# Performance work log

Measured on AMD Instinct MI355X. Metric: run time of the kernel, lower is better.

## Reference

```python
import jax, jax.numpy as jnp
import numpy as np

N = 100000      # nodes
E = 1600000     # edges (unique, no self-loops)
DIN = 128
DOUT = 128


def _make_edges():
    """Unique undirected edges, no self-loops, ring guarantees min degree 2.
    Ensures dense-adjacency semantics == edge-list segment-sum semantics."""
    rng = np.random.default_rng(0)
    ring = np.stack([np.arange(N, dtype=np.int64), (np.arange(N, dtype=np.int64) + 1) % N], axis=1)
    ring = np.sort(ring, axis=1)  # canonical (min,max)
    ring_keys = ring[:, 0] * N + ring[:, 1]
    cand = rng.integers(0, N, size=(3 * E, 2), dtype=np.int64)
    cand = cand[cand[:, 0] != cand[:, 1]]
    cand = np.sort(cand, axis=1)
    keys = cand[:, 0] * N + cand[:, 1]
    _, idx = np.unique(keys, return_index=True)
    cand = cand[np.sort(idx)]
    cand = cand[~np.isin(cand[:, 0] * N + cand[:, 1], ring_keys)][: E - N]
    edges = np.concatenate([ring, cand], axis=0)  # [E, 2]
    return edges.T  # [2, E]


def setup_inputs() -> dict:
    key = jax.random.key(0)
    kx, kw = jax.random.split(key)
    X = jax.random.normal(kx, (N, DIN), dtype=jnp.float32)
    # kaiming_normal_ default (fan_in mode): std = sqrt(2 / fan_in)
    W = jax.random.normal(kw, (DIN, DOUT), dtype=jnp.float32) * np.float32(np.sqrt(2.0 / DIN))
    edge_list = jnp.asarray(_make_edges(), dtype=jnp.int64)
    return {"X": X, "W": W, "edge_list": edge_list}


def reference(X, W, edge_list):
    src, dst = edge_list[0], edge_list[1]
    n = X.shape[0]
    ones = jnp.ones(src.shape[0], dtype=X.dtype)
    # D: each edge increments both endpoint degrees (matches the torch loop)
    deg = jnp.zeros((n,), X.dtype).at[src].add(ones).at[dst].add(ones)
    # A_hat @ X = symmetric neighbor aggregation + self (identity)
    agg = jnp.zeros_like(X).at[dst].add(X[src]).at[src].add(X[dst]) + X
    # D^-1 is inverse of diagonal -> elementwise reciprocal
    z = (agg / deg[:, None]) @ W
    return jax.nn.relu(z)
```

## Files before the change

kernel.cpp:

```cpp
#include <hip/hip_runtime.h>
#include <hip/hip_fp16.h>


#define DFEAT 128
#define BSH 7
#define BNODES (1 << BSH)
#define NBMAX 800
#define EPB 8192
#define SORT_CAP 6144

typedef __attribute__((ext_vector_type(8))) short short8;
typedef __attribute__((ext_vector_type(4))) float f32x4;

__device__ __forceinline__ unsigned short f2bf(float x) {
  unsigned u = __float_as_uint(x);
  return (unsigned short)((u + 0x7FFFu + ((u >> 16) & 1u)) >> 16);
}
__device__ __forceinline__ __half2 u2h(unsigned x) {
  union { unsigned u; __half2 h; } c; c.u = x; return c.h;
}

__global__ void init_kernel(const int* el32, int* gcur, int* flag, int NB) {
  int i = blockIdx.x * blockDim.x + threadIdx.x;
  if (i < NB) gcur[i] = 0;
  if (i == 0) flag[0] = (el32[1] == 0 && el32[3] == 0) ? 1 : 0;
}

__device__ __forceinline__ int edge_at(const void* el, long long i, int mode64) {
  if (mode64) return (int)((const long long*)el)[i];
  return ((const int*)el)[i];
}

__global__ __launch_bounds__(1024) void scatter_kernel(const void* el,
                                                       const int* __restrict__ flag,
                                                       int* __restrict__ gcur,
                                                       unsigned int* __restrict__ bucket,
                                                       int E, int NB) {
  __shared__ int lh[NBMAX];
  __shared__ int lb[NBMAX];
  int t = threadIdx.x;
  for (int i = t; i < NB; i += 1024) lh[i] = 0;
  __syncthreads();
  int m = flag[0];
  long long e0 = (long long)blockIdx.x * EPB + t;
  int s[8], d[8];
#pragma unroll
  for (int r = 0; r < 8; r++) {
    long long e = e0 + r * 1024;
    if (e < E) {
      s[r] = edge_at(el, e, m);
      d[r] = edge_at(el, (long long)E + e, m);
    } else {
      s[r] = -1;
    }
  }
#pragma unroll
  for (int r = 0; r < 8; r++) {
    if (s[r] >= 0) {
      atomicAdd(&lh[s[r] >> BSH], 1);
      atomicAdd(&lh[d[r] >> BSH], 1);
    }
  }
  __syncthreads();
  for (int i = t; i < NB; i += 1024) {
    int c = lh[i];
    lb[i] = c ? atomicAdd(&gcur[i], c) : 0;
  }
  __syncthreads();
  for (int i = t; i < NB; i += 1024) lh[i] = 0;
  __syncthreads();
#pragma unroll
  for (int r = 0; r < 8; r++) {
    if (s[r] >= 0) {
      int bs = s[r] >> BSH, bd = d[r] >> BSH;
      int ps = lb[bs] + atomicAdd(&lh[bs], 1);
      if (ps < SORT_CAP)
        bucket[(long long)bs * SORT_CAP + ps] =
            ((unsigned)(s[r] & (BNODES - 1)) << 20) | (unsigned)d[r];
      int pd = lb[bd] + atomicAdd(&lh[bd], 1);
      if (pd < SORT_CAP)
        bucket[(long long)bd * SORT_CAP + pd] =
            ((unsigned)(d[r] & (BNODES - 1)) << 20) | (unsigned)s[r];
    }
  }
}

__global__ __launch_bounds__(1024) void sort_kernel(const unsigned int* __restrict__ bucket,
                                                    const int* __restrict__ gcur,
                                                    int* __restrict__ adj,
                                                    int* __restrict__ start,
                                                    int* __restrict__ degg,
                                                    int n) {
  __shared__ int srt[SORT_CAP];
  __shared__ int h[BNODES], pref[BNODES], cur[BNODES], scn[BNODES];
  int b = blockIdx.x, t = threadIdx.x;
  int cnt = gcur[b]; if (cnt > SORT_CAP) cnt = SORT_CAP;
  long long base = (long long)b * SORT_CAP;

  if (t < BNODES) h[t] = 0;
  __syncthreads();
  for (int i = t; i < cnt; i += 1024)
    atomicAdd(&h[bucket[base + i] >> 20], 1);
  __syncthreads();
  int v = (t < BNODES) ? h[t] : 0;
  if (t < BNODES) scn[t] = v;
  __syncthreads();
  for (int dd = 1; dd < BNODES; dd <<= 1) {
    int a = (t < BNODES && t >= dd) ? scn[t - dd] : 0;
    __syncthreads();
    if (t < BNODES) scn[t] += a;
    __syncthreads();
  }
  if (t < BNODES) { pref[t] = scn[t] - v; cur[t] = scn[t] - v; }
  __syncthreads();
  for (int i = t; i < cnt; i += 1024) {
    unsigned e = bucket[base + i];
    int p = atomicAdd(&cur[e >> 20], 1);
    srt[p] = (int)(e & 0xFFFFFu);
  }
  __syncthreads();
  for (int i = t; i < cnt; i += 1024) adj[base + i] = srt[i];
  int node = (b << BSH) + t;
  if (t < BNODES && node < n) {
    start[node] = (int)(base + pref[t]);
    degg[node] = h[t];
  }
}

__global__ __launch_bounds__(256) void wfrag_kernel(const float* __restrict__ W,
                                                    unsigned int* __restrict__ Wfrag) {
  int e = blockIdx.x * 256 + threadIdx.x;
  if (e >= 2048) return;
  int lane = e & 63;
  int nt = (e >> 6) & 7;
  int kc = e >> 9;
  int k0 = kc * 32 + (lane >> 4) * 8;
  int col = nt * 16 + (lane & 15);
  unsigned int o[4];
#pragma unroll
  for (int jj = 0; jj < 4; jj++) {
    unsigned short lo = f2bf(W[(k0 + 2 * jj) * DFEAT + col]);
    unsigned short hi = f2bf(W[(k0 + 2 * jj + 1) * DFEAT + col]);
    o[jj] = (unsigned)lo | ((unsigned)hi << 16);
  }
  uint4* dst = (uint4*)Wfrag;
  uint4 v; v.x = o[0]; v.y = o[1]; v.z = o[2]; v.w = o[3];
  dst[e] = v;
}

__global__ __launch_bounds__(256) void gemm_kernel(const float* __restrict__ X,
                                                   const short8* __restrict__ Wfrag,
                                                   __half* __restrict__ Yh, int n) {
  int wave = threadIdx.x >> 6;
  int lane = threadIdx.x & 63;
  int row0 = (blockIdx.x * 4 + wave) * 16;
  if (row0 >= n) return;

  int rowA = row0 + (lane & 15);
  if (rowA >= n) rowA = n - 1;
  const float4* Xrow = (const float4*)(X + (long long)rowA * DFEAT);
  int koff = (lane >> 4) * 2;

  f32x4 acc[8];
#pragma unroll
  for (int ntp = 0; ntp < 8; ntp++) acc[ntp] = (f32x4){0.f, 0.f, 0.f, 0.f};

#pragma unroll
  for (int kc = 0; kc < 4; kc++) {
    float4 xa = Xrow[kc * 8 + koff];
    float4 xb = Xrow[kc * 8 + koff + 1];
    short8 a8;
    a8[0] = (short)f2bf(xa.x); a8[1] = (short)f2bf(xa.y);
    a8[2] = (short)f2bf(xa.z); a8[3] = (short)f2bf(xa.w);
    a8[4] = (short)f2bf(xb.x); a8[5] = (short)f2bf(xb.y);
    a8[6] = (short)f2bf(xb.z); a8[7] = (short)f2bf(xb.w);
#pragma unroll
    for (int nt = 0; nt < 8; nt++) {
      short8 b8 = Wfrag[(kc * 8 + nt) * 64 + lane];
      acc[nt] = __builtin_amdgcn_mfma_f32_16x16x32_bf16(a8, b8, acc[nt], 0, 0, 0);
    }
  }

  int rbase = row0 + (lane >> 4) * 4;
  int cbase = lane & 15;
#pragma unroll
  for (int nt = 0; nt < 8; nt++) {
#pragma unroll
    for (int r = 0; r < 4; r++) {
      int row = rbase + r;
      if (row < n)
        Yh[(long long)row * DFEAT + nt * 16 + cbase] = __float2half(acc[nt][r]);
    }
  }
}

__global__ __launch_bounds__(256) void gather_kernel(const unsigned int* __restrict__ Yh,
                                                     const int* __restrict__ start,
                                                     const int* __restrict__ degg,
                                                     const int* __restrict__ adj,
                                                     float2* __restrict__ out2, int n) {
  int wid = (int)((blockIdx.x * (long long)blockDim.x + threadIdx.x) >> 6);
  int lane = threadIdx.x & 63;
  if (wid >= n) return;

  int off0 = start[wid], len = degg[wid];
  __half2 acc0 = u2h(Yh[(long long)wid * 64 + lane]);
  __half2 acc1 = u2h(0);

  for (int base = 0; base < len; base += 64) {
    int cnt = len - base; if (cnt > 64) cnt = 64;
    int idx = (lane < cnt) ? adj[off0 + base + lane] : 0;
    int t = 0;
    for (; t + 8 <= cnt; t += 8) {
      unsigned v[8];
#pragma unroll
      for (int u = 0; u < 8; u++) {
        int j = __shfl(idx, t + u);
        v[u] = Yh[(long long)j * 64 + lane];
      }
      acc0 = __hadd2(acc0, u2h(v[0])); acc1 = __hadd2(acc1, u2h(v[1]));
      acc0 = __hadd2(acc0, u2h(v[2])); acc1 = __hadd2(acc1, u2h(v[3]));
      acc0 = __hadd2(acc0, u2h(v[4])); acc1 = __hadd2(acc1, u2h(v[5]));
      acc0 = __hadd2(acc0, u2h(v[6])); acc1 = __hadd2(acc1, u2h(v[7]));
    }
    for (; t < cnt; t++) {
      int j = __shfl(idx, t);
      acc0 = __hadd2(acc0, u2h(Yh[(long long)j * 64 + lane]));
    }
  }

  float2 f0 = __half22float2(acc0);
  float2 f1 = __half22float2(acc1);
  float inv = 1.0f / (float)len;
  float2 o;
  o.x = (f0.x + f1.x) * inv;
  o.y = (f0.y + f1.y) * inv;
  o.x = o.x > 0.f ? o.x : 0.f;
  o.y = o.y > 0.f ? o.y : 0.f;
  out2[(long long)wid * 64 + lane] = o;
}

extern "C" void kernel_launch(void* const* d_in, const int* in_sizes, int n_in,
                              void* d_out, int out_size, void* d_ws, size_t ws_size,
                              hipStream_t stream) {
  const float* X = (const float*)d_in[0];
  const float* W = (const float*)d_in[1];
  const void* el = d_in[2];
  float* out = (float*)d_out;

  int n = in_sizes[0] / DFEAT;
  int E = in_sizes[2] / 2;
  int NB = (n + BNODES - 1) >> BSH;

  char* p = (char*)d_ws;
  auto alloc = [&](size_t bytes) -> char* {
    char* q = p;
    p += (bytes + 511) & ~(size_t)511;
    return q;
  };
  int* gcur = (int*)alloc((size_t)NBMAX * 4);
  int* flag = (int*)alloc(64);
  unsigned int* bucket = (unsigned int*)alloc((size_t)NBMAX * SORT_CAP * 4);
  int* adj   = (int*)alloc((size_t)NBMAX * SORT_CAP * 4);
  int* start = (int*)alloc((size_t)n * 4);
  int* degg  = (int*)alloc((size_t)n * 4);
  unsigned int* Wfrag = (unsigned int*)alloc((size_t)2048 * 16);
  __half* Yh = (__half*)alloc((size_t)n * DFEAT * 2);

  int eblocks = (E + EPB - 1) / EPB;

  init_kernel<<<(NBMAX + 255) / 256, 256, 0, stream>>>((const int*)el, gcur, flag, NB);
  scatter_kernel<<<eblocks, 1024, 0, stream>>>(el, flag, gcur, bucket, E, NB);
  sort_kernel<<<NB, 1024, 0, stream>>>(bucket, gcur, adj, start, degg, n);
  wfrag_kernel<<<8, 256, 0, stream>>>(W, Wfrag);
  gemm_kernel<<<(n + 63) / 64, 256, 0, stream>>>(X, (const short8*)Wfrag, Yh, n);
  gather_kernel<<<(n + 3) / 4, 256, 0, stream>>>((const unsigned int*)Yh, start, degg,
                                                 adj, (float2*)out, n);
}
```

Before: 267.0 us.

## Split Y into feature slices and gather per slice for cache locality

The GEMM now writes Y as eight feature-sliced planes of 16 halfs per row instead of row-major 128-wide rows. The gather runs eight passes, one per slice, with each wave handling 8 neighbors at a time across lane groups and then reducing with cross-lane shuffles. The aim is to shrink the random-access working set per pass (each plane is 3.2 MB) so neighbor rows stay in L2/MALL. In exchange it reads 32-byte segments instead of 256-byte rows, rereads adjacency and degree data eight times, and adds shuffle reductions.

```diff
diff --git a/kernel.cpp b/kernel.cpp
--- a/kernel.cpp
+++ b/kernel.cpp
@@ -8,6 +8,8 @@
 #define NBMAX 800
 #define EPB 8192
 #define SORT_CAP 6144
+#define NSLICE 8
+#define SFEAT 16
 
 typedef __attribute__((ext_vector_type(8))) short short8;
 typedef __attribute__((ext_vector_type(4))) float f32x4;
@@ -18,6 +20,9 @@
 }
 __device__ __forceinline__ __half2 u2h(unsigned x) {
   union { unsigned u; __half2 h; } c; c.u = x; return c.h;
+}
+__device__ __forceinline__ unsigned h2u(__half2 x) {
+  union { __half2 h; unsigned u; } c; c.h = x; return c.u;
 }
 
 __global__ void init_kernel(const int* el32, int* gcur, int* flag, int NB) {
@@ -185,11 +190,12 @@
   int cbase = lane & 15;
 #pragma unroll
   for (int nt = 0; nt < 8; nt++) {
+    __half* Ys = Yh + (long long)nt * n * SFEAT;
 #pragma unroll
     for (int r = 0; r < 4; r++) {
       int row = rbase + r;
       if (row < n)
-        Yh[(long long)row * DFEAT + nt * 16 + cbase] = __float2half(acc[nt][r]);
+        Ys[(long long)row * SFEAT + cbase] = __float2half(acc[nt][r]);
     }
   }
 }
@@ -198,46 +204,60 @@
                                                      const int* __restrict__ start,
                                                      const int* __restrict__ degg,
                                                      const int* __restrict__ adj,
-                                                     float2* __restrict__ out2, int n) {
-  int wid = (int)((blockIdx.x * (long long)blockDim.x + threadIdx.x) >> 6);
+                                                     float* __restrict__ out,
+                                                     int n, int bps) {
+  int slice = blockIdx.x / bps;
+  int nb = blockIdx.x % bps;
+  int wave = threadIdx.x >> 6;
+  int wid = nb * 4 + wave;
+  if (wid >= n) return;
   int lane = threadIdx.x & 63;
-  if (wid >= n) return;
-
+  int g = lane >> 3, fl = lane & 7;
+
+  const unsigned int* Ys = Yh + (long long)slice * n * (SFEAT / 2);
   int off0 = start[wid], len = degg[wid];
-  __half2 acc0 = u2h(Yh[(long long)wid * 64 + lane]);
+
+  __half2 acc0 = u2h(g == 0 ? Ys[(long long)wid * 8 + fl] : 0u);
   __half2 acc1 = u2h(0);
 
   for (int base = 0; base < len; base += 64) {
     int cnt = len - base; if (cnt > 64) cnt = 64;
     int idx = (lane < cnt) ? adj[off0 + base + lane] : 0;
     int t = 0;
-    for (; t + 8 <= cnt; t += 8) {
-      unsigned v[8];
-#pragma unroll
-      for (int u = 0; u < 8; u++) {
-        int j = __shfl(idx, t + u);
-        v[u] = Yh[(long long)j * 64 + lane];
-      }
-      acc0 = __hadd2(acc0, u2h(v[0])); acc1 = __hadd2(acc1, u2h(v[1]));
-      acc0 = __hadd2(acc0, u2h(v[2])); acc1 = __hadd2(acc1, u2h(v[3]));
-      acc0 = __hadd2(acc0, u2h(v[4])); acc1 = __hadd2(acc1, u2h(v[5]));
-      acc0 = __hadd2(acc0, u2h(v[6])); acc1 = __hadd2(acc1, u2h(v[7]));
-    }
-    for (; t < cnt; t++) {
-      int j = __shfl(idx, t);
-      acc0 = __hadd2(acc0, u2h(Yh[(long long)j * 64 + lane]));
-    }
-  }
-
-  float2 f0 = __half22float2(acc0);
-  float2 f1 = __half22float2(acc1);
-  float inv = 1.0f / (float)len;
-  float2 o;
-  o.x = (f0.x + f1.x) * inv;
-  o.y = (f0.y + f1.y) * inv;
-  o.x = o.x > 0.f ? o.x : 0.f;
-  o.y = o.y > 0.f ? o.y : 0.f;
-  out2[(long long)wid * 64 + lane] = o;
+    for (; t + 32 <= cnt; t += 32) {
+      int j0 = __shfl(idx, t + g);
+      int j1 = __shfl(idx, t + 8 + g);
+      int j2 = __shfl(idx, t + 16 + g);
+      int j3 = __shfl(idx, t + 24 + g);
+      unsigned u0 = Ys[(long long)j0 * 8 + fl];
+      unsigned u1 = Ys[(long long)j1 * 8 + fl];
+      unsigned u2 = Ys[(long long)j2 * 8 + fl];
+      unsigned u3 = Ys[(long long)j3 * 8 + fl];
+      acc0 = __hadd2(acc0, u2h(u0)); acc1 = __hadd2(acc1, u2h(u1));
+      acc0 = __hadd2(acc0, u2h(u2)); acc1 = __hadd2(acc1, u2h(u3));
+    }
+    for (; t < cnt; t += 8) {
+      int j = __shfl(idx, t + g);
+      unsigned u = Ys[(long long)j * 8 + fl];
+      if (t + g < cnt) acc0 = __hadd2(acc0, u2h(u));
+    }
+  }
+
+  __half2 acc = __hadd2(acc0, acc1);
+  acc = __hadd2(acc, u2h((unsigned)__shfl_xor((int)h2u(acc), 8)));
+  acc = __hadd2(acc, u2h((unsigned)__shfl_xor((int)h2u(acc), 16)));
+  acc = __hadd2(acc, u2h((unsigned)__shfl_xor((int)h2u(acc), 32)));
+
+  if (g == 0) {
+    float2 f = __half22float2(acc);
+    float inv = 1.0f / (float)len;
+    float2 o;
+    o.x = f.x * inv; o.y = f.y * inv;
+    o.x = o.x > 0.f ? o.x : 0.f;
+    o.y = o.y > 0.f ? o.y : 0.f;
+    float2* op = (float2*)(out + (long long)wid * DFEAT + slice * SFEAT);
+    op[fl] = o;
+  }
 }
 
 extern "C" void kernel_launch(void* const* d_in, const int* in_sizes, int n_in,
@@ -268,12 +288,13 @@
   __half* Yh = (__half*)alloc((size_t)n * DFEAT * 2);
 
   int eblocks = (E + EPB - 1) / EPB;
+  int bps = (n + 3) / 4;
 
   init_kernel<<<(NBMAX + 255) / 256, 256, 0, stream>>>((const int*)el, gcur, flag, NB);
   scatter_kernel<<<eblocks, 1024, 0, stream>>>(el, flag, gcur, bucket, E, NB);
   sort_kernel<<<NB, 1024, 0, stream>>>(bucket, gcur, adj, start, degg, n);
   wfrag_kernel<<<8, 256, 0, stream>>>(W, Wfrag);
   gemm_kernel<<<(n + 63) / 64, 256, 0, stream>>>(X, (const short8*)Wfrag, Yh, n);
-  gather_kernel<<<(n + 3) / 4, 256, 0, stream>>>((const unsigned int*)Yh, start, degg,
-                                                 adj, (float2*)out, n);
-}
+  gather_kernel<<<bps * NSLICE, 256, 0, stream>>>((const unsigned int*)Yh, start, degg,
+                                                  adj, out, n, bps);
+}
```

Result: slower. 412.8 us (+54.6%).

## Privatize LDS histograms per sub-group in scatter/sort and fuse W prep into init

Applied to the files above, without the earlier changes.

Splits the shared-memory bucket histograms in the scatter and sort kernels into four per-subgroup copies, which cuts LDS atomic contention, and assigns per-subgroup offsets so the ordering stays consistent. The sort kernel now uses 512 threads and caches bucket entries in LDS so they are read from global memory only once. The W-to-bf16 fragment conversion is merged into the init kernel, saving one launch. In exchange, the scatter kernel issues four times as many global atomicAdds on the bucket counters, and both kernels use more LDS.

```diff
diff --git a/kernel.cpp b/kernel.cpp
--- a/kernel.cpp
+++ b/kernel.cpp
@@ -8,6 +8,7 @@
 #define NBMAX 800
 #define EPB 8192
 #define SORT_CAP 6144
+#define NSUB 4
 
 typedef __attribute__((ext_vector_type(8))) short short8;
 typedef __attribute__((ext_vector_type(4))) float f32x4;
@@ -20,10 +21,28 @@
   union { unsigned u; __half2 h; } c; c.u = x; return c.h;
 }
 
-__global__ void init_kernel(const int* el32, int* gcur, int* flag, int NB) {
-  int i = blockIdx.x * blockDim.x + threadIdx.x;
-  if (i < NB) gcur[i] = 0;
-  if (i == 0) flag[0] = (el32[1] == 0 && el32[3] == 0) ? 1 : 0;
+__global__ __launch_bounds__(256) void setup_kernel(const int* el32,
+                                                    const float* __restrict__ W,
+                                                    int* gcur, int* flag,
+                                                    unsigned int* __restrict__ Wfrag) {
+  int id = blockIdx.x * 256 + threadIdx.x;
+  if (id < NBMAX) gcur[id] = 0;
+  if (id == 0) flag[0] = (el32[1] == 0 && el32[3] == 0) ? 1 : 0;
+
+  int lane = id & 63;
+  int nt = (id >> 6) & 7;
+  int kc = id >> 9;
+  int k0 = kc * 32 + (lane >> 4) * 8;
+  int col = nt * 16 + (lane & 15);
+  unsigned int o[4];
+#pragma unroll
+  for (int jj = 0; jj < 4; jj++) {
+    unsigned short lo = f2bf(W[(k0 + 2 * jj) * DFEAT + col]);
+    unsigned short hi = f2bf(W[(k0 + 2 * jj + 1) * DFEAT + col]);
+    o[jj] = (unsigned)lo | ((unsigned)hi << 16);
+  }
+  uint4 v; v.x = o[0]; v.y = o[1]; v.z = o[2]; v.w = o[3];
+  ((uint4*)Wfrag)[id] = v;
 }
 
 __device__ __forceinline__ int edge_at(const void* el, long long i, int mode64) {
@@ -36,10 +55,11 @@
                                                        int* __restrict__ gcur,
                                                        unsigned int* __restrict__ bucket,
                                                        int E, int NB) {
-  __shared__ int lh[NBMAX];
-  __shared__ int lb[NBMAX];
+  __shared__ int lh[NSUB][NBMAX];
+  __shared__ int lb[NSUB][NBMAX];
   int t = threadIdx.x;
-  for (int i = t; i < NB; i += 1024) lh[i] = 0;
+  int sub = t >> 8;
+  for (int i = t; i < NSUB * NBMAX; i += 1024) (&lh[0][0])[i] = 0;
   __syncthreads();
   int m = flag[0];
   long long e0 = (long long)blockIdx.x * EPB + t;
@@ -57,27 +77,30 @@
 #pragma unroll
   for (int r = 0; r < 8; r++) {
     if (s[r] >= 0) {
-      atomicAdd(&lh[s[r] >> BSH], 1);
-      atomicAdd(&lh[d[r] >> BSH], 1);
-    }
-  }
-  __syncthreads();
-  for (int i = t; i < NB; i += 1024) {
-    int c = lh[i];
-    lb[i] = c ? atomicAdd(&gcur[i], c) : 0;
-  }
-  __syncthreads();
-  for (int i = t; i < NB; i += 1024) lh[i] = 0;
+      atomicAdd(&lh[sub][s[r] >> BSH], 1);
+      atomicAdd(&lh[sub][d[r] >> BSH], 1);
+    }
+  }
+  __syncthreads();
+  for (int i = t; i < NSUB * NB; i += 1024) {
+    int ss = i >> 10;
+    ss = i / NB;
+    int bb = i - ss * NB;
+    int c = lh[ss][bb];
+    lb[ss][bb] = c ? atomicAdd(&gcur[bb], c) : 0;
+  }
+  __syncthreads();
+  for (int i = t; i < NSUB * NBMAX; i += 1024) (&lh[0][0])[i] = 0;
   __syncthreads();
 #pragma unroll
   for (int r = 0; r < 8; r++) {
     if (s[r] >= 0) {
       int bs = s[r] >> BSH, bd = d[r] >> BSH;
-      int ps = lb[bs] + atomicAdd(&lh[bs], 1);
+      int ps = lb[sub][bs] + atomicAdd(&lh[sub][bs], 1);
       if (ps < SORT_CAP)
         bucket[(long long)bs * SORT_CAP + ps] =
             ((unsigned)(s[r] & (BNODES - 1)) << 20) | (unsigned)d[r];
-      int pd = lb[bd] + atomicAdd(&lh[bd], 1);
+      int pd = lb[sub][bd] + atomicAdd(&lh[sub][bd], 1);
       if (pd < SORT_CAP)
         bucket[(long long)bd * SORT_CAP + pd] =
             ((unsigned)(d[r] & (BNODES - 1)) << 20) | (unsigned)s[r];
@@ -85,25 +108,35 @@
   }
 }
 
-__global__ __launch_bounds__(1024) void sort_kernel(const unsigned int* __restrict__ bucket,
-                                                    const int* __restrict__ gcur,
-                                                    int* __restrict__ adj,
-                                                    int* __restrict__ start,
-                                                    int* __restrict__ degg,
-                                                    int n) {
+__global__ __launch_bounds__(512) void sort_kernel(const unsigned int* __restrict__ bucket,
+                                                   const int* __restrict__ gcur,
+                                                   int* __restrict__ adj,
+                                                   int* __restrict__ start,
+                                                   int* __restrict__ degg,
+                                                   int n) {
+  __shared__ unsigned ent[SORT_CAP];
   __shared__ int srt[SORT_CAP];
-  __shared__ int h[BNODES], pref[BNODES], cur[BNODES], scn[BNODES];
+  __shared__ int h[NSUB][BNODES];
+  __shared__ int tot[BNODES], pref[BNODES], scn[BNODES];
+  __shared__ int cur[NSUB][BNODES];
   int b = blockIdx.x, t = threadIdx.x;
+  int sub = t >> 7;
   int cnt = gcur[b]; if (cnt > SORT_CAP) cnt = SORT_CAP;
   long long base = (long long)b * SORT_CAP;
 
-  if (t < BNODES) h[t] = 0;
-  __syncthreads();
-  for (int i = t; i < cnt; i += 1024)
-    atomicAdd(&h[bucket[base + i] >> 20], 1);
-  __syncthreads();
-  int v = (t < BNODES) ? h[t] : 0;
-  if (t < BNODES) scn[t] = v;
+  for (int i = t; i < NSUB * BNODES; i += 512) (&h[0][0])[i] = 0;
+  __syncthreads();
+  for (int i = t; i < cnt; i += 512) {
+    unsigned e = bucket[base + i];
+    ent[i] = e;
+    atomicAdd(&h[sub][e >> 20], 1);
+  }
+  __syncthreads();
+  if (t < BNODES) {
+    int s0 = h[0][t], s1 = h[1][t], s2 = h[2][t], s3 = h[3][t];
+    tot[t] = s0 + s1 + s2 + s3;
+    scn[t] = tot[t];
+  }
   __syncthreads();
   for (int dd = 1; dd < BNODES; dd <<= 1) {
     int a = (t < BNODES && t >= dd) ? scn[t - dd] : 0;
@@ -111,41 +144,27 @@
     if (t < BNODES) scn[t] += a;
     __syncthreads();
   }
-  if (t < BNODES) { pref[t] = scn[t] - v; cur[t] = scn[t] - v; }
-  __syncthreads();
-  for (int i = t; i < cnt; i += 1024) {
-    unsigned e = bucket[base + i];
-    int p = atomicAdd(&cur[e >> 20], 1);
+  if (t < BNODES) {
+    int ex = scn[t] - tot[t];
+    pref[t] = ex;
+    cur[0][t] = ex;
+    cur[1][t] = ex + h[0][t];
+    cur[2][t] = ex + h[0][t] + h[1][t];
+    cur[3][t] = ex + h[0][t] + h[1][t] + h[2][t];
+  }
+  __syncthreads();
+  for (int i = t; i < cnt; i += 512) {
+    unsigned e = ent[i];
+    int p = atomicAdd(&cur[sub][e >> 20], 1);
     srt[p] = (int)(e & 0xFFFFFu);
   }
   __syncthreads();
-  for (int i = t; i < cnt; i += 1024) adj[base + i] = srt[i];
+  for (int i = t; i < cnt; i += 512) adj[base + i] = srt[i];
   int node = (b << BSH) + t;
   if (t < BNODES && node < n) {
     start[node] = (int)(base + pref[t]);
-    degg[node] = h[t];
-  }
-}
-
-__global__ __launch_bounds__(256) void wfrag_kernel(const float* __restrict__ W,
-                                                    unsigned int* __restrict__ Wfrag) {
-  int e = blockIdx.x * 256 + threadIdx.x;
-  if (e >= 2048) return;
-  int lane = e & 63;
-  int nt = (e >> 6) & 7;
-  int kc = e >> 9;
-  int k0 = kc * 32 + (lane >> 4) * 8;
-  int col = nt * 16 + (lane & 15);
-  unsigned int o[4];
-#pragma unroll
-  for (int jj = 0; jj < 4; jj++) {
-    unsigned short lo = f2bf(W[(k0 + 2 * jj) * DFEAT + col]);
-    unsigned short hi = f2bf(W[(k0 + 2 * jj + 1) * DFEAT + col]);
-    o[jj] = (unsigned)lo | ((unsigned)hi << 16);
-  }
-  uint4* dst = (uint4*)Wfrag;
-  uint4 v; v.x = o[0]; v.y = o[1]; v.z = o[2]; v.w = o[3];
-  dst[e] = v;
+    degg[node] = tot[t];
+  }
 }
 
 __global__ __launch_bounds__(256) void gemm_kernel(const float* __restrict__ X,
@@ -269,10 +288,9 @@
 
   int eblocks = (E + EPB - 1) / EPB;
 
-  init_kernel<<<(NBMAX + 255) / 256, 256, 0, stream>>>((const int*)el, gcur, flag, NB);
+  setup_kernel<<<8, 256, 0, stream>>>((const int*)el, W, gcur, flag, Wfrag);
   scatter_kernel<<<eblocks, 1024, 0, stream>>>(el, flag, gcur, bucket, E, NB);
-  sort_kernel<<<NB, 1024, 0, stream>>>(bucket, gcur, adj, start, degg, n);
-  wfrag_kernel<<<8, 256, 0, stream>>>(W, Wfrag);
+  sort_kernel<<<NB, 512, 0, stream>>>(bucket, gcur, adj, start, degg, n);
   gemm_kernel<<<(n + 63) / 64, 256, 0, stream>>>(X, (const short8*)Wfrag, Yh, n);
   gather_kernel<<<(n + 3) / 4, 256, 0, stream>>>((const unsigned int*)Yh, start, degg,
                                                  adj, (float2*)out, n);
```

After: 270.7 us. No clear change (+1.4%).

## Fuse W-fragment prep into init and co-schedule sort with GEMM blocks

Applied to the files above, without the earlier changes.

Folds W bf16 fragment packing into the init kernel, and merges the per-bucket sort and the X·W MFMA GEMM into one launch, with separate block ranges so both run concurrently. The sort now stages entries in LDS and writes adj directly instead of through a sorted LDS copy, and uses 512 threads. The gather is split into three launches over node ranges. This cuts launch count and lets the compute-bound GEMM overlap the latency-bound sort. The three-way gather split adds launches with no clear benefit, and the direct scattered adj writes may coalesce worse.

```diff
diff --git a/kernel.cpp b/kernel.cpp
--- a/kernel.cpp
+++ b/kernel.cpp
@@ -20,10 +20,28 @@
   union { unsigned u; __half2 h; } c; c.u = x; return c.h;
 }
 
-__global__ void init_kernel(const int* el32, int* gcur, int* flag, int NB) {
-  int i = blockIdx.x * blockDim.x + threadIdx.x;
-  if (i < NB) gcur[i] = 0;
-  if (i == 0) flag[0] = (el32[1] == 0 && el32[3] == 0) ? 1 : 0;
+__global__ __launch_bounds__(256) void setup_kernel(const int* el32,
+                                                    const float* __restrict__ W,
+                                                    int* gcur, int* flag,
+                                                    unsigned int* __restrict__ Wfrag) {
+  int id = blockIdx.x * 256 + threadIdx.x;
+  if (id < NBMAX) gcur[id] = 0;
+  if (id == 0) flag[0] = (el32[1] == 0 && el32[3] == 0) ? 1 : 0;
+
+  int lane = id & 63;
+  int nt = (id >> 6) & 7;
+  int kc = id >> 9;
+  int k0 = kc * 32 + (lane >> 4) * 8;
+  int col = nt * 16 + (lane & 15);
+  unsigned int o[4];
+#pragma unroll
+  for (int jj = 0; jj < 4; jj++) {
+    unsigned short lo = f2bf(W[(k0 + 2 * jj) * DFEAT + col]);
+    unsigned short hi = f2bf(W[(k0 + 2 * jj + 1) * DFEAT + col]);
+    o[jj] = (unsigned)lo | ((unsigned)hi << 16);
+  }
+  uint4 v; v.x = o[0]; v.y = o[1]; v.z = o[2]; v.w = o[3];
+  ((uint4*)Wfrag)[id] = v;
 }
 
 __device__ __forceinline__ int edge_at(const void* el, long long i, int mode64) {
@@ -85,111 +103,90 @@
   }
 }
 
-__global__ __launch_bounds__(1024) void sort_kernel(const unsigned int* __restrict__ bucket,
-                                                    const int* __restrict__ gcur,
-                                                    int* __restrict__ adj,
-                                                    int* __restrict__ start,
-                                                    int* __restrict__ degg,
-                                                    int n) {
-  __shared__ int srt[SORT_CAP];
+__global__ __launch_bounds__(512) void sortgemm_kernel(
+    const unsigned int* __restrict__ bucket, const int* __restrict__ gcur,
+    int* __restrict__ adj, int* __restrict__ start, int* __restrict__ degg,
+    const float* __restrict__ X, const short8* __restrict__ Wfrag,
+    __half* __restrict__ Yh, int n, int NB) {
+  __shared__ unsigned ent[SORT_CAP];
   __shared__ int h[BNODES], pref[BNODES], cur[BNODES], scn[BNODES];
-  int b = blockIdx.x, t = threadIdx.x;
-  int cnt = gcur[b]; if (cnt > SORT_CAP) cnt = SORT_CAP;
-  long long base = (long long)b * SORT_CAP;
-
-  if (t < BNODES) h[t] = 0;
-  __syncthreads();
-  for (int i = t; i < cnt; i += 1024)
-    atomicAdd(&h[bucket[base + i] >> 20], 1);
-  __syncthreads();
-  int v = (t < BNODES) ? h[t] : 0;
-  if (t < BNODES) scn[t] = v;
-  __syncthreads();
-  for (int dd = 1; dd < BNODES; dd <<= 1) {
-    int a = (t < BNODES && t >= dd) ? scn[t - dd] : 0;
-    __syncthreads();
-    if (t < BNODES) scn[t] += a;
-    __syncthreads();
-  }
-  if (t < BNODES) { pref[t] = scn[t] - v; cur[t] = scn[t] - v; }
-  __syncthreads();
-  for (int i = t; i < cnt; i += 1024) {
-    unsigned e = bucket[base + i];
-    int p = atomicAdd(&cur[e >> 20], 1);
-    srt[p] = (int)(e & 0xFFFFFu);
-  }
-  __syncthreads();
-  for (int i = t; i < cnt; i += 1024) adj[base + i] = srt[i];
-  int node = (b << BSH) + t;
-  if (t < BNODES && node < n) {
-    start[node] = (int)(base + pref[t]);
-    degg[node] = h[t];
-  }
-}
-
-__global__ __launch_bounds__(256) void wfrag_kernel(const float* __restrict__ W,
-                                                    unsigned int* __restrict__ Wfrag) {
-  int e = blockIdx.x * 256 + threadIdx.x;
-  if (e >= 2048) return;
-  int lane = e & 63;
-  int nt = (e >> 6) & 7;
-  int kc = e >> 9;
-  int k0 = kc * 32 + (lane >> 4) * 8;
-  int col = nt * 16 + (lane & 15);
-  unsigned int o[4];
-#pragma unroll
-  for (int jj = 0; jj < 4; jj++) {
-    unsigned short lo = f2bf(W[(k0 + 2 * jj) * DFEAT + col]);
-    unsigned short hi = f2bf(W[(k0 + 2 * jj + 1) * DFEAT + col]);
-    o[jj] = (unsigned)lo | ((unsigned)hi << 16);
-  }
-  uint4* dst = (uint4*)Wfrag;
-  uint4 v; v.x = o[0]; v.y = o[1]; v.z = o[2]; v.w = o[3];
-  dst[e] = v;
-}
-
-__global__ __launch_bounds__(256) void gemm_kernel(const float* __restrict__ X,
-                                                   const short8* __restrict__ Wfrag,
-                                                   __half* __restrict__ Yh, int n) {
-  int wave = threadIdx.x >> 6;
-  int lane = threadIdx.x & 63;
-  int row0 = (blockIdx.x * 4 + wave) * 16;
-  if (row0 >= n) return;
-
-  int rowA = row0 + (lane & 15);
-  if (rowA >= n) rowA = n - 1;
-  const float4* Xrow = (const float4*)(X + (long long)rowA * DFEAT);
-  int koff = (lane >> 4) * 2;
-
-  f32x4 acc[8];
-#pragma unroll
-  for (int ntp = 0; ntp < 8; ntp++) acc[ntp] = (f32x4){0.f, 0.f, 0.f, 0.f};
-
-#pragma unroll
-  for (int kc = 0; kc < 4; kc++) {
-    float4 xa = Xrow[kc * 8 + koff];
-    float4 xb = Xrow[kc * 8 + koff + 1];
-    short8 a8;
-    a8[0] = (short)f2bf(xa.x); a8[1] = (short)f2bf(xa.y);
-    a8[2] = (short)f2bf(xa.z); a8[3] = (short)f2bf(xa.w);
-    a8[4] = (short)f2bf(xb.x); a8[5] = (short)f2bf(xb.y);
-    a8[6] = (short)f2bf(xb.z); a8[7] = (short)f2bf(xb.w);
+
+  if ((int)blockIdx.x < NB) {
+    int b = blockIdx.x, t = threadIdx.x;
+    int cnt = gcur[b]; if (cnt > SORT_CAP) cnt = SORT_CAP;
+    long long base = (long long)b * SORT_CAP;
+
+    if (t < BNODES) h[t] = 0;
+    __syncthreads();
+    for (int i = t; i < cnt; i += 512) {
+      unsigned e = bucket[base + i];
+      ent[i] = e;
+      atomicAdd(&h[e >> 20], 1);
+    }
+    __syncthreads();
+    int v = (t < BNODES) ? h[t] : 0;
+    if (t < BNODES) scn[t] = v;
+    __syncthreads();
+    for (int dd = 1; dd < BNODES; dd <<= 1) {
+      int a = (t < BNODES && t >= dd) ? scn[t - dd] : 0;
+      __syncthreads();
+      if (t < BNODES) scn[t] += a;
+      __syncthreads();
+    }
+    if (t < BNODES) { pref[t] = scn[t] - v; cur[t] = scn[t] - v; }
+    __syncthreads();
+    for (int i = t; i < cnt; i += 512) {
+      unsigned e = ent[i];
+      int p = atomicAdd(&cur[e >> 20], 1);
+      adj[base + p] = (int)(e & 0xFFFFFu);
+    }
+    int node = (b << BSH) + t;
+    if (t < BNODES && node < n) {
+      start[node] = (int)(base + pref[t]);
+      degg[node] = h[t];
+    }
+  } else {
+    int gb = blockIdx.x - NB;
+    int wave = threadIdx.x >> 6;
+    int lane = threadIdx.x & 63;
+    int row0 = (gb * 8 + wave) * 16;
+    if (row0 >= n) return;
+
+    int rowA = row0 + (lane & 15);
+    if (rowA >= n) rowA = n - 1;
+    const float4* Xrow = (const float4*)(X + (long long)rowA * DFEAT);
+    int koff = (lane >> 4) * 2;
+
+    f32x4 acc[8];
+#pragma unroll
+    for (int ntp = 0; ntp < 8; ntp++) acc[ntp] = (f32x4){0.f, 0.f, 0.f, 0.f};
+
+#pragma unroll
+    for (int kc = 0; kc < 4; kc++) {
+      float4 xa = Xrow[kc * 8 + koff];
+      float4 xb = Xrow[kc * 8 + koff + 1];
+      short8 a8;
+      a8[0] = (short)f2bf(xa.x); a8[1] = (short)f2bf(xa.y);
+      a8[2] = (short)f2bf(xa.z); a8[3] = (short)f2bf(xa.w);
+      a8[4] = (short)f2bf(xb.x); a8[5] = (short)f2bf(xb.y);
+      a8[6] = (short)f2bf(xb.z); a8[7] = (short)f2bf(xb.w);
+#pragma unroll
+      for (int nt = 0; nt < 8; nt++) {
+        short8 b8 = Wfrag[(kc * 8 + nt) * 64 + lane];
+        acc[nt] = __builtin_amdgcn_mfma_f32_16x16x32_bf16(a8, b8, acc[nt], 0, 0, 0);
+      }
+    }
+
+    int rbase = row0 + (lane >> 4) * 4;
+    int cbase = lane & 15;
 #pragma unroll
     for (int nt = 0; nt < 8; nt++) {
-      short8 b8 = Wfrag[(kc * 8 + nt) * 64 + lane];
-      acc[nt] = __builtin_amdgcn_mfma_f32_16x16x32_bf16(a8, b8, acc[nt], 0, 0, 0);
-    }
-  }
-
-  int rbase = row0 + (lane >> 4) * 4;
-  int cbase = lane & 15;
-#pragma unroll
-  for (int nt = 0; nt < 8; nt++) {
-#pragma unroll
-    for (int r = 0; r < 4; r++) {
-      int row = rbase + r;
-      if (row < n)
-        Yh[(long long)row * DFEAT + nt * 16 + cbase] = __float2half(acc[nt][r]);
+#pragma unroll
+      for (int r = 0; r < 4; r++) {
+        int row = rbase + r;
+        if (row < n)
+          Yh[(long long)row * DFEAT + nt * 16 + cbase] = __float2half(acc[nt][r]);
+      }
     }
   }
 }
@@ -198,10 +195,11 @@
                                                      const int* __restrict__ start,
                                                      const int* __restrict__ degg,
                                                      const int* __restrict__ adj,
-                                                     float2* __restrict__ out2, int n) {
-  int wid = (int)((blockIdx.x * (long long)blockDim.x + threadIdx.x) >> 6);
+                                                     float2* __restrict__ out2,
+                                                     int nbeg, int nend) {
+  int wid = nbeg + (int)((blockIdx.x * (long long)blockDim.x + threadIdx.x) >> 6);
   int lane = threadIdx.x & 63;
-  if (wid >= n) return;
+  if (wid >= nend) return;
 
   int off0 = start[wid], len = degg[wid];
   __half2 acc0 = u2h(Yh[(long long)wid * 64 + lane]);
@@ -268,12 +266,19 @@
   __half* Yh = (__half*)alloc((size_t)n * DFEAT * 2);
 
   int eblocks = (E + EPB - 1) / EPB;
-
-  init_kernel<<<(NBMAX + 255) / 256, 256, 0, stream>>>((const int*)el, gcur, flag, NB);
+  int gemmblocks = (n + 127) / 128;
+
+  setup_kernel<<<8, 256, 0, stream>>>((const int*)el, W, gcur, flag, Wfrag);
   scatter_kernel<<<eblocks, 1024, 0, stream>>>(el, flag, gcur, bucket, E, NB);
-  sort_kernel<<<NB, 1024, 0, stream>>>(bucket, gcur, adj, start, degg, n);
-  wfrag_kernel<<<8, 256, 0, stream>>>(W, Wfrag);
-  gemm_kernel<<<(n + 63) / 64, 256, 0, stream>>>(X, (const short8*)Wfrag, Yh, n);
-  gather_kernel<<<(n + 3) / 4, 256, 0, stream>>>((const unsigned int*)Yh, start, degg,
-                                                 adj, (float2*)out, n);
-}
+  sortgemm_kernel<<<NB + gemmblocks, 512, 0, stream>>>(
+      bucket, gcur, adj, start, degg, X, (const short8*)Wfrag, Yh, n, NB);
+
+  int np = (n + 2) / 3;
+  for (int k = 0; k < 3; k++) {
+    int nbeg = k * np;
+    int nend = (k == 2) ? n : (k + 1) * np;
+    int blocks = ((nend - nbeg) + 3) / 4;
+    gather_kernel<<<blocks, 256, 0, stream>>>((const unsigned int*)Yh, start, degg,
+                                              adj, (float2*)out, nbeg, nend);
+  }
+}
```

Result: slower. 283.0 us (+6.0%).
